# Performance work log

Hardware: AMD Instinct MI355X
Metric: run time of the kernel (lower is better)

## Reference

```python
import jax, jax.numpy as jnp
import numpy as np

N, E, B = 20000, 100000, 16
U_SZ, U_RED = 4096, 256
EDGE_H, EDGE_OUT = 1024, 512
NODE_H = 512
X_DIM, EA_DIM = 9, 1


def _lin(key, fan_out, fan_in):
    kw, kb = jax.random.split(key)
    s = 1.0 / np.sqrt(fan_in)
    w = jax.random.uniform(kw, (fan_out, fan_in), jnp.float32, -s, s)
    b = jax.random.uniform(kb, (fan_out,), jnp.float32, -s, s)
    return w, b


def setup_inputs() -> dict:
    key = jax.random.key(0)
    ks = jax.random.split(key, 16)
    inp = {}
    inp["x"] = jax.random.normal(ks[0], (N, X_DIM), jnp.float32)
    inp["edge_index"] = jax.random.randint(ks[1], (2, E), 0, N, jnp.int64)
    inp["edge_attr"] = jax.random.normal(ks[2], (E, EA_DIM), jnp.float32)
    inp["u"] = jax.random.normal(ks[3], (B, U_SZ), jnp.float32)
    inp["batch"] = jnp.sort(jax.random.randint(ks[4], (N,), 0, B, jnp.int64))
    # select_dim_reduction: Linear(4096, 256)
    inp["w_sel"], inp["b_sel"] = _lin(ks[5], U_RED, U_SZ)
    # edge MLP: 275 -> 1024 -> 1024 -> 1024 -> 1024 -> 512
    e_in = EA_DIM + 2 * X_DIM + U_RED  # 275
    inp["ew0"], inp["eb0"] = _lin(ks[6], EDGE_H, e_in)
    inp["ew1"], inp["eb1"] = _lin(ks[7], EDGE_H, EDGE_H)
    inp["ew2"], inp["eb2"] = _lin(ks[8], EDGE_H, EDGE_H)
    inp["ew3"], inp["eb3"] = _lin(ks[9], EDGE_H, EDGE_H)
    inp["ew4"], inp["eb4"] = _lin(ks[10], EDGE_OUT, EDGE_H)
    # node_mlp_1: (9+512) -> 512 -> 512 (relu after each)
    inp["nw0"], inp["nb0"] = _lin(ks[11], NODE_H, X_DIM + EDGE_OUT)
    inp["nw1"], inp["nb1"] = _lin(ks[12], NODE_H, NODE_H)
    # node_mlp_2: (9+512+256) -> 512 -> 1
    inp["mw0"], inp["mb0"] = _lin(ks[13], NODE_H, X_DIM + NODE_H + U_RED)
    inp["mw1"], inp["mb1"] = _lin(ks[14], 1, NODE_H)
    return inp


def reference(x, edge_index, edge_attr, u, batch,
              w_sel, b_sel,
              ew0, eb0, ew1, eb1, ew2, eb2, ew3, eb3, ew4, eb4,
              nw0, nb0, nw1, nb1, mw0, mb0, mw1, mb1):
    row, col = edge_index[0], edge_index[1]
    u_r = u @ w_sel.T + b_sel                       # [B, 256]
    eb_idx = batch[row]                             # edge -> graph
    # EdgeModel: cat([src, dest, edge_attr, u[batch]]) -> MLP
    e_in = jnp.concatenate([x[row], x[col], edge_attr, u_r[eb_idx]], axis=1)  # [E,275]
    h = jax.nn.relu(e_in @ ew0.T + eb0)
    h = jax.nn.relu(h @ ew1.T + eb1)
    h = jax.nn.relu(h @ ew2.T + eb2)
    h = jax.nn.relu(h @ ew3.T + eb3)
    edge_out = h @ ew4.T + eb4                      # [E, 512]
    # NodeModel: gather x[col], edge MLP, scatter_mean onto row
    n_in = jnp.concatenate([x[col], edge_out], axis=1)  # [E, 521]
    h = jax.nn.relu(n_in @ nw0.T + nb0)
    h = jax.nn.relu(h @ nw1.T + nb1)                # [E, 512]
    seg_sum = jax.ops.segment_sum(h, row, num_segments=x.shape[0])
    cnt = jax.ops.segment_sum(jnp.ones((h.shape[0],), h.dtype), row, num_segments=x.shape[0])
    agg = seg_sum / jnp.maximum(cnt, 1.0)[:, None]  # scatter_mean
    m_in = jnp.concatenate([x, agg, u_r[batch]], axis=1)  # [N, 777]
    h2 = jax.nn.relu(m_in @ mw0.T + mb0)
    out = h2 @ mw1.T + mb1                          # [N, 1]
    return jnp.squeeze(out)
```

## Files before the change

kernel.cpp:

```cpp
#include <hip/hip_runtime.h>


#define NN 20000
#define EE 100000
#define BB 16

typedef _Float16 f16x8 __attribute__((ext_vector_type(8)));
typedef _Float16 f16x4 __attribute__((ext_vector_type(4)));
typedef float f32x4 __attribute__((ext_vector_type(4)));

__device__ __forceinline__ int clampi(int v, int hi) {
    return v < 0 ? 0 : (v >= hi ? hi - 1 : v);
}

__device__ __forceinline__ void gld_lds16(const void* g, void* l) {
    __builtin_amdgcn_global_load_lds(
        (const __attribute__((address_space(1))) unsigned int*)g,
        (__attribute__((address_space(3))) unsigned int*)l, 16, 0, 0);
}

__device__ __forceinline__ void bar_lgkm() {
    asm volatile("s_waitcnt lgkmcnt(0)" ::: "memory");
    __builtin_amdgcn_s_barrier();
}

__global__ __launch_bounds__(256, 2) void gemm256h(
    const _Float16* __restrict__ Ag, const _Float16* __restrict__ Wt,
    int KT, int KTs, const float* __restrict__ bias,
    _Float16* __restrict__ C, int KTo, int ktOff)
{
    __shared__ _Float16 smem[24576];

    const int tid  = threadIdx.x;
    const int lane = tid & 63;
    const int wid  = tid >> 6;
    const int wm   = wid & 1;
    const int wn   = wid >> 1;
    const int l15  = lane & 15;
    const int l4   = (lane >> 4) << 2;
    const int kq   = (lane >> 4) << 10;

    const int nb  = gridDim.x;
    const int MT2 = gridDim.y;
    int f = blockIdx.y * nb + blockIdx.x;
    const int MT8 = MT2 & ~7;
    int p, c;
    if (f < MT8 * nb) {
        c = (f >> 3) % nb;
        p = (f & 7) + 8 * ((f >> 3) / nb);
    } else {
        int g = f - MT8 * nb;
        p = MT8 + g / nb;
        c = g % nb;
    }

    const int S = KT;
    auto stage = [&](int ph) {
        const _Float16* gA0 = Ag + ((size_t)(2 * p)     * KTs + ph) * 4096 + tid * 8;
        const _Float16* gA1 = Ag + ((size_t)(2 * p + 1) * KTs + ph) * 4096 + tid * 8;
        const _Float16* gB  = Wt + ((size_t)c * KT + ph) * 4096 + tid * 8;
        _Float16* rA = smem + (ph & 1) * 12288;
        _Float16* rB = rA + 8192;
        gld_lds16(gA0,        rA + wid * 512);
        gld_lds16(gA0 + 2048, rA + 2048 + wid * 512);
        gld_lds16(gA1,        rA + 4096 + wid * 512);
        gld_lds16(gA1 + 2048, rA + 6144 + wid * 512);
        gld_lds16(gB,         rB + wid * 512);
        gld_lds16(gB + 2048,  rB + 2048 + wid * 512);
    };

    f32x4 acc[8][4];
#pragma unroll
    for (int i = 0; i < 8; ++i)
#pragma unroll
        for (int j = 0; j < 4; ++j) acc[i][j] = (f32x4){0.f, 0.f, 0.f, 0.f};

    stage(0);

    for (int s = 0; s < S; ++s) {
        asm volatile("s_waitcnt vmcnt(0)" ::: "memory");
        __builtin_amdgcn_s_barrier();
        if (s + 1 < S) stage(s + 1);
        const _Float16* rA = smem + (s & 1) * 12288;
        const _Float16* rB = rA + 8192;
        const _Float16* Ap = rA + wm * 4096 + kq + l15 * 8;
        const _Float16* Bp = rB + kq + wn * 512 + l15 * 8;
        f16x8 af[8], bf[4];
#pragma unroll
        for (int j = 0; j < 4; ++j) bf[j] = *(const f16x8*)(Bp + j * 128);
#pragma unroll
        for (int i = 0; i < 8; ++i) af[i] = *(const f16x8*)(Ap + i * 128);
        __builtin_amdgcn_s_setprio(1);
#pragma unroll
        for (int i = 0; i < 8; ++i)
#pragma unroll
            for (int j = 0; j < 4; ++j)
                acc[i][j] = __builtin_amdgcn_mfma_f32_16x16x32_f16(
                    af[i], bf[j], acc[i][j], 0, 0, 0);
        __builtin_amdgcn_s_setprio(0);
    }

    _Float16* tr = smem;
#pragma unroll
    for (int pass = 0; pass < 4; ++pass) {
        bar_lgkm();
        if (wm == (pass >> 1)) {
            const int fi = (pass & 1) << 2;
#pragma unroll
            for (int i = 0; i < 4; ++i) {
#pragma unroll
                for (int v = 0; v < 4; ++v) {
                    const int lr = i * 16 + l4 + v;
#pragma unroll
                    for (int j = 0; j < 4; ++j) {
                        const int cc = wn * 64 + j * 16 + l15;
                        float val = acc[fi + i][j][v] + bias[c * 128 + cc];
                        val = fmaxf(val, 0.f);
                        tr[lr * 132 + cc] = (_Float16)val;
                    }
                }
            }
        }
        bar_lgkm();
#pragma unroll
        for (int it = 0; it < 4; ++it) {
            const int id = it * 256 + tid;
            const int r  = id & 63;
            const int cg = id >> 6;
            f16x4 lo = *(const f16x4*)(tr + r * 132 + cg * 8);
            f16x4 hi = *(const f16x4*)(tr + r * 132 + cg * 8 + 4);
            f16x8 v8;
#pragma unroll
            for (int t = 0; t < 4; ++t) { v8[t] = lo[t]; v8[t + 4] = hi[t]; }
            const int kti = ktOff + (c << 2) + (cg >> 2);
            const int mt_out = 2 * p + (pass >> 1);
            const int r128 = ((pass & 1) << 6) + r;
            *(f16x8*)(C + (((size_t)mt_out * KTo + kti) * 4 + (cg & 3)) * 1024
                        + (size_t)r128 * 8) = v8;
        }
    }
}

__global__ __launch_bounds__(256, 3) void gemmAD(
    const _Float16* __restrict__ Ag, const _Float16* __restrict__ Wt,
    int KT, int KTs, const float* __restrict__ bias,
    _Float16* __restrict__ C, int KTo, int ktOff)
{
    __shared__ _Float16 As[16384];

    const int tid  = threadIdx.x;
    const int lane = tid & 63;
    const int wid  = tid >> 6;
    const int wm = (wid & 1) << 6;
    const int wn = (wid >> 1) << 6;
    const int l15 = lane & 15;
    const int l4  = (lane >> 4) << 2;
    const int kg  = (lane >> 4) << 10;

    const int nb = gridDim.x;
    const int MT = gridDim.y;
    int f = blockIdx.y * nb + blockIdx.x;
    const int MT8 = MT & ~7;
    int p, c;
    if (f < MT8 * nb) {
        c = (f >> 3) % nb;
        p = (f & 7) + 8 * ((f >> 3) / nb);
    } else {
        int g = f - MT8 * nb;
        p = MT8 + g / nb;
        c = g % nb;
    }

    f32x4 acc[4][4];
#pragma unroll
    for (int i = 0; i < 4; ++i)
#pragma unroll
        for (int j = 0; j < 4; ++j) acc[i][j] = (f32x4){0.f, 0.f, 0.f, 0.f};

    const _Float16* gA = Ag + (size_t)p * KTs * 4096;
    const _Float16* gB = Wt + ((size_t)c * KT) * 4096 + kg + (wn + l15) * 8;
    const int ktLim = KT - 1;

    auto stageA = [&](int ktA) {
        const _Float16* s = gA + (size_t)ktA * 4096 + tid * 8;
        _Float16* d = As + ((ktA & 3) << 12) + wid * 512;
        gld_lds16(s, d);
        gld_lds16(s + 2048, d + 2048);
    };

    f16x8 bfA[4], bfB[4];
    auto loadB = [&](f16x8 (&bf)[4], int ktB) {
        const _Float16* bp = gB + (size_t)ktB * 4096;
#pragma unroll
        for (int j = 0; j < 4; ++j) bf[j] = *(const f16x8*)(bp + j * 128);
    };

    stageA(0);
    stageA(1 <= ktLim ? 1 : ktLim);
    loadB(bfA, 0);

    auto body = [&](int kt, f16x8 (&cur)[4], f16x8 (&nxt)[4]) {
        const int ktB = kt + 1 <= ktLim ? kt + 1 : ktLim;
        const int ktA = kt + 2 <= ktLim ? kt + 2 : ktLim;
        loadB(nxt, ktB);
        stageA(ktA);
        asm volatile("s_waitcnt vmcnt(12)" ::: "memory");
        __builtin_amdgcn_s_barrier();
        asm volatile("" ::: "memory");
        const _Float16* Ap = As + ((kt & 3) << 12) + kg + (wm + l15) * 8;
        f16x8 af[4];
#pragma unroll
        for (int i = 0; i < 4; ++i) af[i] = *(const f16x8*)(Ap + i * 128);
        __builtin_amdgcn_s_setprio(1);
#pragma unroll
        for (int i = 0; i < 4; ++i)
#pragma unroll
            for (int j = 0; j < 4; ++j)
                acc[i][j] = __builtin_amdgcn_mfma_f32_16x16x32_f16(
                    af[i], cur[j], acc[i][j], 0, 0, 0);
        __builtin_amdgcn_s_setprio(0);
    };

    for (int kt = 0; kt + 2 <= KT; kt += 2) {
        body(kt,     bfA, bfB);
        body(kt + 1, bfB, bfA);
    }
    if (KT & 1) body(KT - 1, bfA, bfB);

    _Float16* tr = As;
#pragma unroll
    for (int pass = 0; pass < 2; ++pass) {
        if (pass == 0) __syncthreads(); else bar_lgkm();
        if (wm == pass * 64) {
#pragma unroll
            for (int i = 0; i < 4; ++i) {
#pragma unroll
                for (int v = 0; v < 4; ++v) {
                    const int lr = i * 16 + l4 + v;
#pragma unroll
                    for (int j = 0; j < 4; ++j) {
                        const int cc = wn + j * 16 + l15;
                        float val = acc[i][j][v] + bias[c * 128 + cc];
                        val = fmaxf(val, 0.f);
                        tr[lr * 132 + cc] = (_Float16)val;
                    }
                }
            }
        }
        bar_lgkm();
#pragma unroll
        for (int it = 0; it < 4; ++it) {
            const int id = it * 256 + tid;
            const int r  = id & 63;
            const int cg = id >> 6;
            f16x4 lo = *(const f16x4*)(tr + r * 132 + cg * 8);
            f16x4 hi = *(const f16x4*)(tr + r * 132 + cg * 8 + 4);
            f16x8 v8;
#pragma unroll
            for (int t = 0; t < 4; ++t) { v8[t] = lo[t]; v8[t + 4] = hi[t]; }
            const int kti = ktOff + (c << 2) + (cg >> 2);
            const int gr  = pass * 64 + r;
            size_t o = (((size_t)p * KTo + kti) * 4 + (cg & 3)) * 1024 + (size_t)gr * 8;
            *(f16x8*)(C + o) = v8;
        }
    }
}

template <int MODE>
__global__ __launch_bounds__(256, 4) void gemm_blk(
    const _Float16* __restrict__ A,
    const _Float16* __restrict__ Wt,
    int KT, int KTs,
    const float* __restrict__ bias, int ldbias, const int* __restrict__ gbid,
    void* __restrict__ C, int KTo, int ktOff,
    int ldc,
    const int* __restrict__ srow, float* __restrict__ aux,
    int M, int relu)
{
    __shared__ char smem[32768];
    _Float16* As = (_Float16*)smem;
    _Float16* Bs = As + 8192;

    const int tid  = threadIdx.x;
    const int lane = tid & 63;
    const int wid  = tid >> 6;
    const int wm = (wid & 1) << 6;
    const int wn = (wid >> 1) << 6;

    const int nb = gridDim.x;
    const int MT = gridDim.y;
    int f = blockIdx.y * nb + blockIdx.x;
    const int MT8 = MT & ~7;
    int p, c;
    if (f < MT8 * nb) {
        c = (f >> 3) % nb;
        p = (f & 7) + 8 * ((f >> 3) / nb);
    } else {
        int g = f - MT8 * nb;
        p = MT8 + g / nb;
        c = g % nb;
    }

    f32x4 acc[4][4];
#pragma unroll
    for (int i = 0; i < 4; ++i)
#pragma unroll
        for (int j = 0; j < 4; ++j) acc[i][j] = (f32x4){0.f, 0.f, 0.f, 0.f};

    const _Float16* pA = A + (size_t)p * KTs * 4096;
    const _Float16* pB = Wt + (size_t)c * KT * 4096;
    const int cb0 = wid * 64;
    const int cb1 = 256 + wid * 64;
    const int kq  = (lane >> 4) * 128;
    const int l15 = lane & 15;
    const int l4  = (lane >> 4) << 2;

    int kt = 0;
    for (; kt + 2 <= KT; kt += 2) {
        __syncthreads();
        gld_lds16(pA + (size_t)(cb0 + lane) * 8,        As + cb0 * 8);
        gld_lds16(pA + (size_t)(cb1 + lane) * 8,        As + cb1 * 8);
        gld_lds16(pA + 4096 + (size_t)(cb0 + lane) * 8, As + 4096 + cb0 * 8);
        gld_lds16(pA + 4096 + (size_t)(cb1 + lane) * 8, As + 4096 + cb1 * 8);
        gld_lds16(pB + (size_t)(cb0 + lane) * 8,        Bs + cb0 * 8);
        gld_lds16(pB + (size_t)(cb1 + lane) * 8,        Bs + cb1 * 8);
        gld_lds16(pB + 4096 + (size_t)(cb0 + lane) * 8, Bs + 4096 + cb0 * 8);
        gld_lds16(pB + 4096 + (size_t)(cb1 + lane) * 8, Bs + 4096 + cb1 * 8);
        pA += 8192; pB += 8192;
        __syncthreads();

#pragma unroll
        for (int s = 0; s < 2; ++s) {
            f16x8 af[4], bf[4];
            const int sb = s * 4096;
#pragma unroll
            for (int i = 0; i < 4; ++i)
                af[i] = *(const f16x8*)(As + sb + (size_t)((kq + wm + i * 16 + l15) << 3));
#pragma unroll
            for (int j = 0; j < 4; ++j)
                bf[j] = *(const f16x8*)(Bs + sb + (size_t)((kq + wn + j * 16 + l15) << 3));
#pragma unroll
            for (int i = 0; i < 4; ++i)
#pragma unroll
                for (int j = 0; j < 4; ++j)
                    acc[i][j] = __builtin_amdgcn_mfma_f32_16x16x32_f16(af[i], bf[j], acc[i][j], 0, 0, 0);
        }
    }
    if (kt < KT) {
        __syncthreads();
        gld_lds16(pA + (size_t)(cb0 + lane) * 8, As + cb0 * 8);
        gld_lds16(pA + (size_t)(cb1 + lane) * 8, As + cb1 * 8);
        gld_lds16(pB + (size_t)(cb0 + lane) * 8, Bs + cb0 * 8);
        gld_lds16(pB + (size_t)(cb1 + lane) * 8, Bs + cb1 * 8);
        __syncthreads();
        f16x8 af[4], bf[4];
#pragma unroll
        for (int i = 0; i < 4; ++i)
            af[i] = *(const f16x8*)(As + (size_t)((kq + wm + i * 16 + l15) << 3));
#pragma unroll
        for (int j = 0; j < 4; ++j)
            bf[j] = *(const f16x8*)(Bs + (size_t)((kq + wn + j * 16 + l15) << 3));
#pragma unroll
        for (int i = 0; i < 4; ++i)
#pragma unroll
            for (int j = 0; j < 4; ++j)
                acc[i][j] = __builtin_amdgcn_mfma_f32_16x16x32_f16(af[i], bf[j], acc[i][j], 0, 0, 0);
    }

    if (MODE == 0) {
        _Float16* tr = (_Float16*)smem;
#pragma unroll
        for (int pass = 0; pass < 2; ++pass) {
            bar_lgkm();
            if (wm == pass * 64) {
#pragma unroll
                for (int i = 0; i < 4; ++i) {
#pragma unroll
                    for (int v = 0; v < 4; ++v) {
                        const int lr = i * 16 + l4 + v;
                        const float* brow = bias;
                        if (gbid) {
                            int m = p * 128 + pass * 64 + lr;
                            if (m >= M) m = M - 1;
                            brow = bias + (size_t)clampi(gbid[m], BB) * ldbias;
                        }
#pragma unroll
                        for (int j = 0; j < 4; ++j) {
                            const int cc = wn + j * 16 + l15;
                            float val = acc[i][j][v] + brow[c * 128 + cc];
                            if (relu) val = fmaxf(val, 0.f);
                            tr[lr * 132 + cc] = (_Float16)val;
                        }
                    }
                }
            }
            bar_lgkm();
#pragma unroll
            for (int it = 0; it < 4; ++it) {
                const int id = it * 256 + tid;
                const int r  = id & 63;
                const int cg = id >> 6;
                f16x4 lo = *(const f16x4*)(tr + r * 132 + cg * 8);
                f16x4 hi = *(const f16x4*)(tr + r * 132 + cg * 8 + 4);
                f16x8 v8;
#pragma unroll
                for (int t = 0; t < 4; ++t) { v8[t] = lo[t]; v8[t + 4] = hi[t]; }
                const int kti = ktOff + (c << 2) + (cg >> 2);
                const int gr  = pass * 64 + r;
                size_t o = (((size_t)p * KTo + kti) * 4 + (cg & 3)) * 1024 + (size_t)gr * 8;
                *(f16x8*)((_Float16*)C + o) = v8;
            }
        }
    } else if (MODE == 1) {
#pragma unroll
        for (int i = 0; i < 4; ++i) {
#pragma unroll
            for (int v = 0; v < 4; ++v) {
                const int m = p * 128 + wm + i * 16 + l4 + v;
                if (m >= M) continue;
                const float* brow = bias;
                if (gbid) brow = bias + (size_t)clampi(gbid[m], BB) * ldbias;
#pragma unroll
                for (int j = 0; j < 4; ++j) {
                    const int col = c * 128 + wn + j * 16 + l15;
                    float val = acc[i][j][v] + brow[col];
                    if (relu) val = fmaxf(val, 0.f);
                    ((float*)C)[(size_t)m * ldc + col] = val;
                }
            }
        }
    } else if (MODE == 2) {
        float* trf = (float*)smem;
#pragma unroll
        for (int pass = 0; pass < 4; ++pass) {
            bar_lgkm();
            if (wm == ((pass >> 1) << 6)) {
                const int i0 = (pass & 1) << 1;
#pragma unroll
                for (int ii = 0; ii < 2; ++ii) {
                    const int i = i0 + ii;
                    const int lr = ii * 16 + l4;
#pragma unroll
                    for (int v = 0; v < 4; ++v) {
#pragma unroll
                        for (int j = 0; j < 4; ++j) {
                            const int cc = wn + j * 16 + l15;
                            float val = acc[i][j][v] + bias[c * 128 + cc];
                            if (relu) val = fmaxf(val, 0.f);
                            trf[(lr + v) * 130 + cc] = val;
                        }
                    }
                }
            }
            bar_lgkm();
            const int ebase = p * 128 + pass * 32;
#pragma unroll
            for (int it = 0; it < 16; ++it) {
                const int id = it * 256 + tid;
                const int lr = id >> 7;
                const int colg = id & 127;
                const int el = ebase + lr;
                if (el < M) {
                    const int node = clampi(srow[el], NN);
                    atomicAdd(&aux[(size_t)node * 512 + c * 128 + colg],
                              trf[lr * 130 + colg]);
                }
            }
        }
    } else {
        const float* mw1 = aux;
        float* out = (float*)C;
#pragma unroll
        for (int i = 0; i < 4; ++i) {
#pragma unroll
            for (int v = 0; v < 4; ++v) {
                const int m = p * 128 + wm + i * 16 + l4 + v;
                const int mc = m < M ? m : M - 1;
                const float* brow = bias + (size_t)clampi(gbid[mc], BB) * ldbias;
                float s = 0.f;
#pragma unroll
                for (int j = 0; j < 4; ++j) {
                    const int col = c * 128 + wn + j * 16 + l15;
                    float val = acc[i][j][v] + brow[col];
                    val = fmaxf(val, 0.f);
                    s += val * mw1[col];
                }
                s += __shfl_down(s, 8, 16);
                s += __shfl_down(s, 4, 16);
                s += __shfl_down(s, 2, 16);
                s += __shfl_down(s, 1, 16);
                if (l15 == 0 && m < M) atomicAdd(&out[m], s);
            }
        }
    }
}


__global__ void k_w2h_blk(const float* __restrict__ src, _Float16* __restrict__ dst,
                          int N, int Ksrc, int Kd, int mode)
{
    int t = blockIdx.x * blockDim.x + threadIdx.x;
    if (t >= N * Kd) return;
    int n = t / Kd, k = t - n * Kd;
    float v = 0.f;
    if (mode == 0)      { if (k < Ksrc) v = src[(size_t)n * Ksrc + k]; }
    else if (mode == 1) { if (k < 19) v = src[(size_t)n * 275 + k]; }
    else if (mode == 2) { if (k < 9) v = src[(size_t)n * Ksrc + k];
                          else if (k >= 32 && k < 544) v = src[(size_t)n * Ksrc + 9 + (k - 32)]; }
    else if (mode == 4) { if (k < Ksrc) v = src[(size_t)k * N + n]; }
    else                { v = src[(size_t)n * Ksrc + 9 + k]; }
    int KT = Kd >> 5;
    int nt = n >> 7, r = n & 127, kt = k >> 5, kg = (k >> 3) & 3, ko = k & 7;
    dst[(((size_t)nt * KT + kt) * 4 + kg) * 1024 + (size_t)r * 8 + ko] = (_Float16)v;
}

__global__ void k_fill_w32(const float* __restrict__ nw0, _Float16* __restrict__ whnc)
{
    int t = blockIdx.x * blockDim.x + threadIdx.x;
    if (t >= 512 * 32) return;
    int n = t >> 5, k = t & 31;
    float v = (k < 9) ? nw0[(size_t)n * 521 + k] : 0.f;
    int nt = n >> 7, r = n & 127, kg = (k >> 3) & 3, ko = k & 7;
    whnc[(((size_t)nt * 33 + 32) * 4 + kg) * 1024 + (size_t)r * 8 + ko] = (_Float16)v;
}

__global__ void k_bfuse(const float* __restrict__ nw0, const float* __restrict__ eb4,
                        const float* __restrict__ nb0, float* __restrict__ bf)
{
    int wave = (blockIdx.x * 256 + threadIdx.x) >> 6;
    int lane = threadIdx.x & 63;
    if (wave >= 512) return;
    const float* wr = nw0 + (size_t)wave * 521 + 9;
    float s = 0.f;
#pragma unroll
    for (int i = 0; i < 8; ++i) s += wr[lane * 8 + i] * eb4[lane * 8 + i];
    for (int off = 32; off; off >>= 1) s += __shfl_down(s, off);
    if (lane == 0) bf[wave] = s + nb0[wave];
}

__global__ void k_u_r(const float* __restrict__ u, const float* __restrict__ w_sel,
                      const float* __restrict__ b_sel, float* __restrict__ u_r)
{
    int wave = (blockIdx.x * 256 + threadIdx.x) >> 6;
    int lane = threadIdx.x & 63;
    int b = wave >> 8, n = wave & 255;
    const float4* u4 = (const float4*)(u + (size_t)b * 4096);
    const float4* w4 = (const float4*)(w_sel + (size_t)n * 4096);
    float s = 0.f;
    for (int i = lane; i < 1024; i += 64) {
        float4 a = u4[i], c = w4[i];
        s += a.x * c.x + a.y * c.y + a.z * c.z + a.w * c.w;
    }
    for (int off = 32; off; off >>= 1) s += __shfl_down(s, off);
    if (lane == 0) u_r[b * 256 + n] = s + b_sel[n];
}

__global__ void k_graph_bias(const float* __restrict__ u_r, const float* __restrict__ w,
                             const float* __restrict__ b, float* __restrict__ ub,
                             int Nout, int Ksrc, int koff)
{
    int wave = (blockIdx.x * 256 + threadIdx.x) >> 6;
    int lane = threadIdx.x & 63;
    if (wave >= 16 * Nout) return;
    int g = wave / Nout, n = wave - g * Nout;
    const float* ur = u_r + (size_t)g * 256;
    const float* wr = w + (size_t)n * Ksrc + koff;
    float s = 0.f;
#pragma unroll
    for (int i = 0; i < 4; ++i) s += ur[lane * 4 + i] * wr[lane * 4 + i];
    for (int off = 32; off; off >>= 1) s += __shfl_down(s, off);
    if (lane == 0) ub[(size_t)g * Nout + n] = s + b[n];
}

__global__ void k_gbe(const int* __restrict__ row, const int* __restrict__ batch,
                      int* __restrict__ gbe, float* __restrict__ cnt)
{
    int e = blockIdx.x * blockDim.x + threadIdx.x;
    if (e >= EE) return;
    int r = clampi(row[e], NN);
    gbe[e] = clampi(batch[r], BB);
    atomicAdd(&cnt[r], 1.f);
}

__global__ void k_init_out(float* __restrict__ out, const float* __restrict__ mb1)
{
    int t = blockIdx.x * blockDim.x + threadIdx.x;
    if (t < NN) out[t] = mb1[0];
}

__global__ void k_gather_edge_blk(const float* __restrict__ x, const float* __restrict__ ea,
                                  const int* __restrict__ row, const int* __restrict__ col,
                                  _Float16* __restrict__ dst, _Float16* __restrict__ pong,
                                  int e0, int ec, int MTR)
{
    int t = blockIdx.x * blockDim.x + threadIdx.x;
    if (t >= MTR * 4) return;
    int r = t >> 2, kg = t & 3;
    int e = e0 + r; int emax = e0 + ec - 1;
    if (e > emax) e = emax;
    int ri = clampi(row[e], NN), ci = clampi(col[e], NN);
    f16x8 v;
    f16x8 vx = (f16x8)(_Float16)0.f;
#pragma unroll
    for (int j = 0; j < 8; ++j) {
        int cc = kg * 8 + j;
        float fv = 0.f;
        if (cc < 9)       fv = x[(size_t)ri * 9 + cc];
        else if (cc < 18) fv = x[(size_t)ci * 9 + (cc - 9)];
        else if (cc == 18) fv = ea[e];
        v[j] = (_Float16)fv;
        if (cc < 9) vx[j] = (_Float16)x[(size_t)ci * 9 + cc];
    }
    *(f16x8*)(dst + (size_t)(r >> 7) * 4096 + (size_t)kg * 1024 + (size_t)(r & 127) * 8) = v;
    *(f16x8*)(pong + (((size_t)(r >> 7) * 33 + 32) * 4 + kg) * 1024 + (size_t)(r & 127) * 8) = vx;
}

__global__ void k_gather_min(const float* __restrict__ x, const float* __restrict__ agg,
                             const float* __restrict__ cnt, _Float16* __restrict__ dst, int MTR)
{
    int t = blockIdx.x * blockDim.x + threadIdx.x;
    if (t >= MTR * 68) return;
    int r = t / 68, q = t - r * 68;
    int kt = q >> 2, kg = q & 3;
    int n = r < NN ? r : NN - 1;
    f16x8 v = (f16x8)(_Float16)0.f;
    if (kt == 0) {
#pragma unroll
        for (int j = 0; j < 8; ++j) {
            int cc = kg * 8 + j;
            if (cc < 9) v[j] = (_Float16)x[(size_t)n * 9 + cc];
        }
    } else {
        float inv = 1.f / fmaxf(cnt[n], 1.f);
        int cbase = (kt - 1) * 32 + kg * 8;
        const float4* ap = (const float4*)(agg + (size_t)n * 512 + cbase);
        float4 a0 = ap[0], a1 = ap[1];
        v[0] = (_Float16)(a0.x * inv); v[1] = (_Float16)(a0.y * inv);
        v[2] = (_Float16)(a0.z * inv); v[3] = (_Float16)(a0.w * inv);
        v[4] = (_Float16)(a1.x * inv); v[5] = (_Float16)(a1.y * inv);
        v[6] = (_Float16)(a1.z * inv); v[7] = (_Float16)(a1.w * inv);
    }
    *(f16x8*)(dst + ((size_t)(r >> 7) * 17 + kt) * 4096 + (size_t)kg * 1024 + (size_t)(r & 127) * 8) = v;
}


#define GRID1(n) dim3(((n) + 255) / 256)

static inline void gemmB0(hipStream_t s, const _Float16* A, const _Float16* Wt, int KT, int KTs,
                          const float* bias, int ldbias, const int* gbid,
                          void* C, int KTo, int ktOff,
                          int M, int MT, int NT, int relu)
{
    hipLaunchKernelGGL(gemm_blk<0>, dim3(NT, MT), dim3(256), 0, s,
                       A, Wt, KT, KTs, bias, ldbias, gbid, C, KTo, ktOff, 0,
                       nullptr, nullptr, M, relu);
}
static inline void gemmB2(hipStream_t s, const _Float16* A, const _Float16* Wt, int KT, int KTs,
                          const float* bias, const int* srow, float* agg,
                          int M, int MT, int NT, int relu)
{
    hipLaunchKernelGGL(gemm_blk<2>, dim3(NT, MT), dim3(256), 0, s,
                       A, Wt, KT, KTs, bias, 0, nullptr, nullptr, 0, 0, 0,
                       srow, agg, M, relu);
}
static inline void gemmB3(hipStream_t s, const _Float16* A, const _Float16* Wt, int KT, int KTs,
                          const float* bias, int ldbias, const int* gbid,
                          float* out, const float* mw1,
                          int M, int MT, int NT)
{
    hipLaunchKernelGGL(gemm_blk<3>, dim3(NT, MT), dim3(256), 0, s,
                       A, Wt, KT, KTs, bias, ldbias, gbid, out, 0, 0, 0,
                       nullptr, (float*)mw1, M, 1);
}

extern "C" void kernel_launch(void* const* d_in, const int* in_sizes, int n_in,
                              void* d_out, int out_size, void* d_ws, size_t ws_size,
                              hipStream_t stream)
{
    const float* x     = (const float*)d_in[0];
    const int*   ei    = (const int*)d_in[1];
    const float* ea    = (const float*)d_in[2];
    const float* u     = (const float*)d_in[3];
    const int*   batch = (const int*)d_in[4];
    const float* w_sel = (const float*)d_in[5];
    const float* b_sel = (const float*)d_in[6];
    const float* ew0 = (const float*)d_in[7];   const float* eb0 = (const float*)d_in[8];
    const float* ew1 = (const float*)d_in[9];   const float* eb1 = (const float*)d_in[10];
    const float* ew2 = (const float*)d_in[11];  const float* eb2 = (const float*)d_in[12];
    const float* ew3 = (const float*)d_in[13];  const float* eb3 = (const float*)d_in[14];
    const float* ew4 = (const float*)d_in[15];  const float* eb4 = (const float*)d_in[16];
    const float* nw0 = (const float*)d_in[17];  const float* nb0 = (const float*)d_in[18];
    const float* nw1 = (const float*)d_in[19];  const float* nb1 = (const float*)d_in[20];
    const float* mw0 = (const float*)d_in[21];  const float* mb0 = (const float*)d_in[22];
    const float* mw1 = (const float*)d_in[23];  const float* mb1 = (const float*)d_in[24];

    const int* row = ei;
    const int* col = ei + EE;

    char* W = (char*)d_ws;
    size_t off = 0;
    auto alloc = [&](size_t bytes) -> char* {
        char* p = W + off;
        off = (off + bytes + 255) & ~(size_t)255;
        return p;
    };
    float*    cnt   = (float*)alloc(20000 * 4);
    float*    agg   = (float*)alloc((size_t)NN * 512 * 4);
    float*    zbias = (float*)alloc(1024 * 4);
    const size_t zeroBytes = off;
    float*    u_r  = (float*)alloc(16 * 256 * 4);
    float*    ub0  = (float*)alloc(16 * 1024 * 4);
    float*    ubm  = (float*)alloc(16 * 512 * 4);
    float*    bfu  = (float*)alloc(512 * 4);
    int*      gbe  = (int*)alloc((size_t)EE * 4);
    _Float16* wh0   = (_Float16*)alloc((size_t)8 * 1 * 4096 * 2);
    _Float16* wh1   = (_Float16*)alloc((size_t)8 * 32 * 4096 * 2);
    _Float16* wh2   = (_Float16*)alloc((size_t)8 * 32 * 4096 * 2);
    _Float16* wh3   = (_Float16*)alloc((size_t)8 * 32 * 4096 * 2);
    _Float16* whnc  = (_Float16*)alloc((size_t)4 * 33 * 4096 * 2);
    _Float16* whn1  = (_Float16*)alloc((size_t)4 * 16 * 4096 * 2);
    _Float16* whm0  = (_Float16*)alloc((size_t)4 * 17 * 4096 * 2);
    _Float16* nw0eoB= (_Float16*)alloc((size_t)4 * 16 * 4096 * 2);
    _Float16* ew4T  = (_Float16*)alloc((size_t)8 * 16 * 4096 * 2);
    const int MTm = (NN + 127) / 128;
    _Float16* m_in = (_Float16*)alloc((size_t)MTm * 17 * 4096 * 2);
    const size_t fixedBytes = off;

    static const int ecOpts[] = {32768, 25000, 12500, 10000, 5000};
    int EC = 5000;
    for (int i = 0; i < 5; ++i) {
        int ec = ecOpts[i];
        size_t MTRc = (size_t)((ec + 255) / 256) * 256;
        size_t need = fixedBytes + MTRc * 64 + 2 * (MTRc * 2112) + 4096;
        if (need <= ws_size) { EC = ec; break; }
    }
    const bool big = (EC == 32768);
    const size_t MTR = (size_t)((EC + 255) / 256) * 256;
    _Float16* e_in = (_Float16*)alloc(MTR * 64);
    _Float16* ping = (_Float16*)alloc(MTR * 2112);
    _Float16* pong = (_Float16*)alloc(MTR * 2112);
    const int NCH = (EE + EC - 1) / EC;

    (void)hipMemsetAsync(W, 0, zeroBytes, stream);
    hipLaunchKernelGGL(k_init_out, GRID1(NN), dim3(256), 0, stream, (float*)d_out, mb1);

    hipLaunchKernelGGL(k_u_r, dim3(1024), dim3(256), 0, stream, u, w_sel, b_sel, u_r);
    hipLaunchKernelGGL(k_graph_bias, GRID1(16 * 1024 * 64), dim3(256), 0, stream,
                       u_r, ew0, eb0, ub0, 1024, 275, 19);
    hipLaunchKernelGGL(k_graph_bias, GRID1(16 * 512 * 64), dim3(256), 0, stream,
                       u_r, mw0, mb0, ubm, 512, 777, 521);
    hipLaunchKernelGGL(k_gbe, GRID1(EE), dim3(256), 0, stream, row, batch, gbe, cnt);
    hipLaunchKernelGGL(k_bfuse, dim3(128), dim3(256), 0, stream, nw0, eb4, nb0, bfu);

    auto pack = [&](const float* w, _Float16* wh, int N, int Ksrc, int Kd, int mode) {
        hipLaunchKernelGGL(k_w2h_blk, GRID1(N * Kd), dim3(256), 0, stream, w, wh, N, Ksrc, Kd, mode);
    };
    pack(ew0, wh0, 1024, 275, 32, 1);
    pack(ew1, wh1, 1024, 1024, 1024, 0);
    pack(ew2, wh2, 1024, 1024, 1024, 0);
    pack(ew3, wh3, 1024, 1024, 1024, 0);
    pack(nw1, whn1, 512, 512, 512, 0);
    pack(mw0, whm0, 512, 777, 544, 2);
    pack(nw0, nw0eoB, 512, 521, 512, 5);
    pack(ew4, ew4T, 1024, 512, 512, 4);
    gemmB0(stream, nw0eoB, ew4T, 16, 16, zbias, 0, nullptr, whnc, 33, 0, 512, 4, 8, 0);
    hipLaunchKernelGGL(k_fill_w32, GRID1(512 * 32), dim3(256), 0, stream, nw0, whnc);

    for (int ch = 0; ch < NCH; ++ch) {
        int e0 = ch * EC;
        int ec = EC; if (e0 + ec > EE) ec = EE - e0;
        const int ecr  = ((ec + 255) / 256) * 256;
        const int MTc  = ecr / 128;
        const int MT2c = ecr / 256;
        hipLaunchKernelGGL(k_gather_edge_blk, GRID1(ecr * 4), dim3(256), 0, stream,
                           x, ea, row, col, e_in, pong, e0, ec, ecr);
        gemmB0(stream, e_in, wh0, 1, 1, ub0, 1024, gbe + e0, ping, 33, 0, ec, MTc, 8, 1);
        auto wideL = [&](const _Float16* Ain, const _Float16* Wt,
                         const float* b, _Float16* Cout) {
            if (big)
                hipLaunchKernelGGL(gemm256h, dim3(8, MT2c), dim3(256), 0, stream,
                                   Ain, Wt, 32, 33, b, Cout, 33, 0);
            else
                hipLaunchKernelGGL(gemmAD, dim3(8, MTc), dim3(256), 0, stream,
                                   Ain, Wt, 32, 33, b, Cout, 33, 0);
        };
        wideL(ping, wh1, eb1, pong);
        wideL(pong, wh2, eb2, ping);
        wideL(ping, wh3, eb3, pong);
        hipLaunchKernelGGL(gemmAD, dim3(4, MTc), dim3(256), 0, stream,
                           pong, whnc, 33, 33, bfu, ping, 16, 0);
        gemmB2(stream, ping, whn1, 16, 16, nb1, row + e0, agg, ec, MTc, 4, 1);
    }

    hipLaunchKernelGGL(k_gather_min, GRID1((int)(MTm * 128) * 68), dim3(256), 0, stream,
                       x, agg, cnt, m_in, MTm * 128);
    gemmB3(stream, m_in, whm0, 17, 17, ubm, 512, batch, (float*)d_out, mw1, NN, MTm, 4);
}
```

Measured before the change: 1.422 ms.

## Replace atomic scatter-mean with CSR segmented gather over stored fp16 edge outputs

```diff
diff --git a/kernel.cpp b/kernel.cpp
--- a/kernel.cpp
+++ b/kernel.cpp
@@ -7,6 +7,7 @@
 
 typedef _Float16 f16x8 __attribute__((ext_vector_type(8)));
 typedef _Float16 f16x4 __attribute__((ext_vector_type(4)));
+typedef _Float16 f16x2 __attribute__((ext_vector_type(2)));
 typedef float f32x4 __attribute__((ext_vector_type(4)));
 
 __device__ __forceinline__ int clampi(int v, int hi) {
@@ -467,7 +468,7 @@
                 }
             }
         }
-    } else {
+    } else if (MODE == 3) {
         const float* mw1 = aux;
         float* out = (float*)C;
 #pragma unroll
@@ -490,6 +491,43 @@
                 s += __shfl_down(s, 2, 16);
                 s += __shfl_down(s, 1, 16);
                 if (l15 == 0 && m < M) atomicAdd(&out[m], s);
+            }
+        }
+    } else {
+        _Float16* tr = (_Float16*)smem;
+        _Float16* hout = (_Float16*)C;
+#pragma unroll
+        for (int pass = 0; pass < 2; ++pass) {
+            bar_lgkm();
+            if (wm == pass * 64) {
+#pragma unroll
+                for (int i = 0; i < 4; ++i) {
+#pragma unroll
+                    for (int v = 0; v < 4; ++v) {
+                        const int lr = i * 16 + l4 + v;
+#pragma unroll
+                        for (int j = 0; j < 4; ++j) {
+                            const int cc = wn + j * 16 + l15;
+                            float val = acc[i][j][v] + bias[c * 128 + cc];
+                            if (relu) val = fmaxf(val, 0.f);
+                            tr[lr * 132 + cc] = (_Float16)val;
+                        }
+                    }
+                }
+            }
+            bar_lgkm();
+#pragma unroll
+            for (int it = 0; it < 4; ++it) {
+                const int id = it * 256 + tid;
+                const int cg = id & 15;
+                const int r  = (id >> 4) & 63;
+                f16x4 lo = *(const f16x4*)(tr + r * 132 + cg * 8);
+                f16x4 hi = *(const f16x4*)(tr + r * 132 + cg * 8 + 4);
+                f16x8 v8;
+#pragma unroll
+                for (int t = 0; t < 4; ++t) { v8[t] = lo[t]; v8[t + 4] = hi[t]; }
+                const size_t grow = (size_t)p * 128 + pass * 64 + r;
+                *(f16x8*)(hout + grow * 512 + c * 128 + cg * 8) = v8;
             }
         }
     }
@@ -588,6 +626,81 @@
     if (t < NN) out[t] = mb1[0];
 }
 
+__global__ void k_scan(const float* __restrict__ cnt, int* __restrict__ ptr,
+                       int* __restrict__ cur)
+{
+    __shared__ int part[1024];
+    const int t = threadIdx.x;
+    const int PER = (NN + 1023) / 1024;
+    const int base = t * PER;
+    int s = 0;
+    for (int i = 0; i < PER; ++i) {
+        int n = base + i;
+        if (n < NN) s += (int)cnt[n];
+    }
+    part[t] = s;
+    __syncthreads();
+    for (int off = 1; off < 1024; off <<= 1) {
+        int v = (t >= off) ? part[t - off] : 0;
+        __syncthreads();
+        part[t] += v;
+        __syncthreads();
+    }
+    int run = (t == 0) ? 0 : part[t - 1];
+    for (int i = 0; i < PER; ++i) {
+        int n = base + i;
+        if (n < NN) {
+            ptr[n] = run;
+            cur[n] = run;
+            run += (int)cnt[n];
+        }
+    }
+    if (t == 1023) ptr[NN] = part[1023];
+}
+
+__global__ void k_csr_fill(const int* __restrict__ row, int* __restrict__ cur,
+                           int* __restrict__ idx)
+{
+    int e = blockIdx.x * blockDim.x + threadIdx.x;
+    if (e >= EE) return;
+    int r = clampi(row[e], NN);
+    int pos = atomicAdd(&cur[r], 1);
+    idx[pos] = e;
+}
+
+__global__ void k_gather_csr(const float* __restrict__ x, const _Float16* __restrict__ h,
+                             const int* __restrict__ ptr, const int* __restrict__ idx,
+                             const float* __restrict__ cnt, _Float16* __restrict__ dst)
+{
+    const int n = blockIdx.x;
+    const int t = threadIdx.x;
+    const int base = ptr[n];
+    const int deg = (int)cnt[n];
+    const int c0 = 2 * t;
+    float s0 = 0.f, s1 = 0.f;
+    for (int d = 0; d < deg; ++d) {
+        const int e = idx[base + d];
+        f16x2 hv = *(const f16x2*)(h + (size_t)e * 512 + c0);
+        s0 += (float)hv[0];
+        s1 += (float)hv[1];
+    }
+    const float inv = 1.f / fmaxf(cnt[n], 1.f);
+    const int mt = n >> 7, r = n & 127;
+    const int kt = 1 + (c0 >> 5), kg = (c0 >> 3) & 3, ko = c0 & 7;
+    _Float16* dp = dst + (((size_t)mt * 17 + kt) * 4 + kg) * 1024 + (size_t)r * 8 + ko;
+    f16x2 o; o[0] = (_Float16)(s0 * inv); o[1] = (_Float16)(s1 * inv);
+    *(f16x2*)dp = o;
+    if (t < 16) {
+        const int cx = 2 * t;
+        f16x2 vx;
+        vx[0] = (_Float16)(cx < 9 ? x[(size_t)n * 9 + cx] : 0.f);
+        vx[1] = (_Float16)(cx + 1 < 9 ? x[(size_t)n * 9 + cx + 1] : 0.f);
+        const int kg0 = (cx >> 3) & 3, ko0 = cx & 7;
+        _Float16* d0 = dst + ((size_t)mt * 17 * 4 + kg0) * 1024 + (size_t)r * 8 + ko0;
+        *(f16x2*)d0 = vx;
+    }
+}
+
 __global__ void k_gather_edge_blk(const float* __restrict__ x, const float* __restrict__ ea,
                                   const int* __restrict__ row, const int* __restrict__ col,
                                   _Float16* __restrict__ dst, _Float16* __restrict__ pong,
@@ -671,6 +784,13 @@
     hipLaunchKernelGGL(gemm_blk<3>, dim3(NT, MT), dim3(256), 0, s,
                        A, Wt, KT, KTs, bias, ldbias, gbid, out, 0, 0, 0,
                        nullptr, (float*)mw1, M, 1);
+}
+static inline void gemmB4(hipStream_t s, const _Float16* A, const _Float16* Wt, int KT, int KTs,
+                          const float* bias, _Float16* hout, int M, int MT, int NT)
+{
+    hipLaunchKernelGGL(gemm_blk<4>, dim3(NT, MT), dim3(256), 0, s,
+                       A, Wt, KT, KTs, bias, 0, nullptr, hout, 0, 0, 0,
+                       nullptr, nullptr, M, 1);
 }
 
 extern "C" void kernel_launch(void* const* d_in, const int* in_sizes, int n_in,
@@ -697,6 +817,35 @@
     const int* row = ei;
     const int* col = ei + EE;
 
+    const int MTm = (NN + 127) / 128;
+    const size_t EEp = 100352;
+
+    auto alsz = [](size_t b) { return (b + 255) & ~(size_t)255; };
+    const size_t commonB =
+        alsz(20000 * 4) + alsz(1024 * 4) + alsz(16 * 256 * 4) + alsz(16 * 1024 * 4) +
+        alsz(16 * 512 * 4) + alsz(512 * 4) + alsz((size_t)EE * 4) +
+        alsz((size_t)8 * 4096 * 2) + 3 * alsz((size_t)8 * 32 * 4096 * 2) +
+        alsz((size_t)4 * 33 * 4096 * 2) + alsz((size_t)4 * 16 * 4096 * 2) +
+        alsz((size_t)4 * 17 * 4096 * 2) + alsz((size_t)4 * 16 * 4096 * 2) +
+        alsz((size_t)8 * 16 * 4096 * 2) + alsz((size_t)MTm * 17 * 4096 * 2);
+    const size_t aggB = alsz((size_t)NN * 512 * 4);
+    const size_t csrB = alsz((NN + 2) * 4) + alsz((size_t)NN * 4) +
+                        alsz((size_t)EE * 4) + alsz(EEp * 512 * 2);
+    auto chB = [&](int ec) {
+        size_t Mr = (size_t)((ec + 255) / 256) * 256;
+        return alsz(Mr * 64) + 2 * alsz(Mr * 2112);
+    };
+    const bool csrPath = (commonB + csrB + chB(32768) + 8192 <= ws_size);
+    int EC = 5000;
+    if (csrPath) EC = 32768;
+    else {
+        static const int ecOpts[] = {32768, 25000, 12500, 10000, 5000};
+        for (int i = 0; i < 5; ++i) {
+            if (commonB + aggB + chB(ecOpts[i]) + 8192 <= ws_size) { EC = ecOpts[i]; break; }
+        }
+    }
+    const bool big = (EC == 32768);
+
     char* W = (char*)d_ws;
     size_t off = 0;
     auto alloc = [&](size_t bytes) -> char* {
@@ -704,9 +853,10 @@
         off = (off + bytes + 255) & ~(size_t)255;
         return p;
     };
-    float*    cnt   = (float*)alloc(20000 * 4);
-    float*    agg   = (float*)alloc((size_t)NN * 512 * 4);
-    float*    zbias = (float*)alloc(1024 * 4);
+    float* cnt = (float*)alloc(20000 * 4);
+    float* agg = nullptr;
+    if (!csrPath) agg = (float*)alloc((size_t)NN * 512 * 4);
+    float* zbias = (float*)alloc(1024 * 4);
     const size_t zeroBytes = off;
     float*    u_r  = (float*)alloc(16 * 256 * 4);
     float*    ub0  = (float*)alloc(16 * 1024 * 4);
@@ -722,19 +872,15 @@
     _Float16* whm0  = (_Float16*)alloc((size_t)4 * 17 * 4096 * 2);
     _Float16* nw0eoB= (_Float16*)alloc((size_t)4 * 16 * 4096 * 2);
     _Float16* ew4T  = (_Float16*)alloc((size_t)8 * 16 * 4096 * 2);
-    const int MTm = (NN + 127) / 128;
-    _Float16* m_in = (_Float16*)alloc((size_t)MTm * 17 * 4096 * 2);
-    const size_t fixedBytes = off;
-
-    static const int ecOpts[] = {32768, 25000, 12500, 10000, 5000};
-    int EC = 5000;
-    for (int i = 0; i < 5; ++i) {
-        int ec = ecOpts[i];
-        size_t MTRc = (size_t)((ec + 255) / 256) * 256;
-        size_t need = fixedBytes + MTRc * 64 + 2 * (MTRc * 2112) + 4096;
-        if (need <= ws_size) { EC = ec; break; }
-    }
-    const bool big = (EC == 32768);
+    _Float16* m_in  = (_Float16*)alloc((size_t)MTm * 17 * 4096 * 2);
+    int*      csr_ptr = nullptr; int* csr_cur = nullptr; int* csr_idx = nullptr;
+    _Float16* h_all = nullptr;
+    if (csrPath) {
+        csr_ptr = (int*)alloc((NN + 2) * 4);
+        csr_cur = (int*)alloc((size_t)NN * 4);
+        csr_idx = (int*)alloc((size_t)EE * 4);
+        h_all   = (_Float16*)alloc(EEp * 512 * 2);
+    }
     const size_t MTR = (size_t)((EC + 255) / 256) * 256;
     _Float16* e_in = (_Float16*)alloc(MTR * 64);
     _Float16* ping = (_Float16*)alloc(MTR * 2112);
@@ -751,6 +897,10 @@
                        u_r, mw0, mb0, ubm, 512, 777, 521);
     hipLaunchKernelGGL(k_gbe, GRID1(EE), dim3(256), 0, stream, row, batch, gbe, cnt);
     hipLaunchKernelGGL(k_bfuse, dim3(128), dim3(256), 0, stream, nw0, eb4, nb0, bfu);
+    if (csrPath) {
+        hipLaunchKernelGGL(k_scan, dim3(1), dim3(1024), 0, stream, cnt, csr_ptr, csr_cur);
+        hipLaunchKernelGGL(k_csr_fill, GRID1(EE), dim3(256), 0, stream, row, csr_cur, csr_idx);
+    }
 
     auto pack = [&](const float* w, _Float16* wh, int N, int Ksrc, int Kd, int mode) {
         hipLaunchKernelGGL(k_w2h_blk, GRID1(N * Kd), dim3(256), 0, stream, w, wh, N, Ksrc, Kd, mode);
@@ -789,10 +939,18 @@
         wideL(ping, wh3, eb3, pong);
         hipLaunchKernelGGL(gemmAD, dim3(4, MTc), dim3(256), 0, stream,
                            pong, whnc, 33, 33, bfu, ping, 16, 0);
-        gemmB2(stream, ping, whn1, 16, 16, nb1, row + e0, agg, ec, MTc, 4, 1);
-    }
-
-    hipLaunchKernelGGL(k_gather_min, GRID1((int)(MTm * 128) * 68), dim3(256), 0, stream,
-                       x, agg, cnt, m_in, MTm * 128);
+        if (csrPath)
+            gemmB4(stream, ping, whn1, 16, 16, nb1, h_all + (size_t)e0 * 512, ec, MTc, 4);
+        else
+            gemmB2(stream, ping, whn1, 16, 16, nb1, row + e0, agg, ec, MTc, 4, 1);
+    }
+
+    if (csrPath) {
+        hipLaunchKernelGGL(k_gather_csr, dim3(NN), dim3(256), 0, stream,
+                           x, h_all, csr_ptr, csr_idx, cnt, m_in);
+    } else {
+        hipLaunchKernelGGL(k_gather_min, GRID1((int)(MTm * 128) * 68), dim3(256), 0, stream,
+                           x, agg, cnt, m_in, MTm * 128);
+    }
     gemmB3(stream, m_in, whm0, 17, 17, ubm, 512, batch, (float*)d_out, mw1, NN, MTm, 4);
 }
```

After: 1.395 ms. No clear change (-1.9%).
